# Performance work log

Measured on AMD Instinct MI355X. Metric: run time of the kernel, lower is better.

## Reference

```python
import jax, jax.numpy as jnp
import numpy as np

B, T, D = 16, 1024, 768
H = 12
HD = D // H
MLP = 3072


def _layernorm(x, g, b, eps=1e-5):
    mu = jnp.mean(x, axis=-1, keepdims=True)
    var = jnp.var(x, axis=-1, keepdims=True)
    return (x - mu) * jax.lax.rsqrt(var + eps) * g + b


def setup_inputs() -> dict:
    key = jax.random.key(0)
    ks = jax.random.split(key, 12)
    s_d = 1.0 / np.sqrt(D)
    s_m = 1.0 / np.sqrt(MLP)
    return {
        "x": jax.random.normal(ks[0], (B, T, D), dtype=jnp.float32),
        "Wq": jax.random.uniform(ks[1], (D, D), jnp.float32, -s_d, s_d),
        "bq": jnp.zeros((D,), jnp.float32),
        "Wk": jax.random.uniform(ks[2], (D, D), jnp.float32, -s_d, s_d),
        "bk": jnp.zeros((D,), jnp.float32),
        "Wv": jax.random.uniform(ks[3], (D, D), jnp.float32, -s_d, s_d),
        "bv": jnp.zeros((D,), jnp.float32),
        "Wo": jax.random.uniform(ks[4], (D, D), jnp.float32, -s_d, s_d),
        "bo": jnp.zeros((D,), jnp.float32),
        "ln1_g": jnp.ones((D,), jnp.float32),
        "ln1_b": jnp.zeros((D,), jnp.float32),
        "ln2_g": jnp.ones((D,), jnp.float32),
        "ln2_b": jnp.zeros((D,), jnp.float32),
        "W1": jax.random.uniform(ks[5], (D, MLP), jnp.float32, -s_d, s_d),
        "b1": jnp.zeros((MLP,), jnp.float32),
        "W2": jax.random.uniform(ks[6], (MLP, D), jnp.float32, -s_m, s_m),
        "b2": jnp.zeros((D,), jnp.float32),
    }


def reference(x, Wq, bq, Wk, bk, Wv, bv, Wo, bo, ln1_g, ln1_b, ln2_g, ln2_b, W1, b1, W2, b2):
    h = _layernorm(x, ln1_g, ln1_b)
    # QKV projections -> [B, H, T, HD]
    q = (h @ Wq + bq).reshape(B, T, H, HD).transpose(0, 2, 1, 3)
    k = (h @ Wk + bk).reshape(B, T, H, HD).transpose(0, 2, 1, 3)
    v = (h @ Wv + bv).reshape(B, T, H, HD).transpose(0, 2, 1, 3)
    # NOTE: original divides by sqrt(input_dim), not sqrt(head_dim)
    scores = jnp.einsum('bhtf,bhjf->bhtj', q, k) / jnp.sqrt(jnp.float32(D))
    score = jax.nn.softmax(scores, axis=-1)
    attn = jnp.einsum('bhij,bhjf->bihf', score, v)  # [B, T, H, HD]
    attn_out = attn.reshape(B, T, D) @ Wo + bo
    out = attn_out + x
    h2 = _layernorm(out, ln2_g, ln2_b)
    # MLP: Linear -> GELU -> Linear -> GELU (GELU after 2nd linear is in the source)
    m = jax.nn.gelu(h2 @ W1 + b1, approximate=False)
    m = jax.nn.gelu(m @ W2 + b2, approximate=False)
    return m + out
```

## Files before the change

### kernel.cpp

```cpp
#include <hip/hip_runtime.h>
#include <hip/hip_bf16.h>
#include <math.h>

#define D_MODEL 768
#define T_SEQ   1024
#define B_BATCH 16
#define MLP_DIM 3072
#define M_ROWS  (B_BATCH * T_SEQ)

typedef __attribute__((ext_vector_type(8))) __bf16          bf16x8;
typedef __attribute__((ext_vector_type(4))) __bf16          bf16x4;
typedef __attribute__((ext_vector_type(4))) float           f32x4;

__device__ __forceinline__ float bf2f(unsigned short u) {
  union { unsigned int u; float f; } w; w.u = ((unsigned int)u) << 16; return w.f;
}
__device__ __forceinline__ unsigned short f2bf(float f) {
  union { float f; unsigned int u; } w; w.f = f;
  unsigned int r = (w.u + 0x7fffu + ((w.u >> 16) & 1u)) >> 16;
  return (unsigned short)r;
}
__device__ __forceinline__ float gelu_f(float x) {
  const float a2 = -2.302283f, b2 = -0.102947f;
  return x / (1.0f + exp2f(x * fmaf(b2, x * x, a2)));
}
__device__ __forceinline__ void gload16(const void* g, void* l) {
  __builtin_amdgcn_global_load_lds(
      (const __attribute__((address_space(1))) unsigned int*)g,
      (__attribute__((address_space(3))) unsigned int*)l, 16, 0, 0);
}

__global__ void wtr_k(const float* __restrict__ src,
                      unsigned short* __restrict__ dst, int R, int C) {
  __shared__ float t[32][33];
  const int c0 = blockIdx.x * 32, r0 = blockIdx.y * 32;
  const int tx = threadIdx.x, ty = threadIdx.y;
  #pragma unroll
  for (int j = 0; j < 32; j += 8)
    t[ty + j][tx] = src[(size_t)(r0 + ty + j) * C + (c0 + tx)];
  __syncthreads();
  #pragma unroll
  for (int j = 0; j < 32; j += 8)
    dst[(size_t)(c0 + ty + j) * R + (r0 + tx)] = f2bf(t[tx][ty + j]);
}

__global__ void bcat_k(const float* __restrict__ a, const float* __restrict__ b,
                       const float* __restrict__ c, float* __restrict__ o) {
  const int i = blockIdx.x * 256 + threadIdx.x;
  if (i < 768) { o[i] = a[i]; o[i + 768] = b[i]; o[i + 1536] = c[i]; }
}

template<int SRC_F32>
__global__ __launch_bounds__(256) void ln_k(const void* __restrict__ src,
    const float* __restrict__ g, const float* __restrict__ b,
    unsigned short* __restrict__ out) {
  const int row = blockIdx.x, tid = threadIdx.x;
  const size_t base = (size_t)row * D_MODEL;
  float v[3];
  #pragma unroll
  for (int i = 0; i < 3; ++i) {
    const int c = tid + (i << 8);
    v[i] = SRC_F32 ? ((const float*)src)[base + c]
                   : bf2f(((const unsigned short*)src)[base + c]);
  }
  float s  = v[0] + v[1] + v[2];
  float sq = v[0]*v[0] + v[1]*v[1] + v[2]*v[2];
  #pragma unroll
  for (int m = 32; m; m >>= 1) { s += __shfl_xor(s, m); sq += __shfl_xor(sq, m); }
  __shared__ float ps[4], pq[4];
  if ((tid & 63) == 0) { ps[tid >> 6] = s; pq[tid >> 6] = sq; }
  __syncthreads();
  s  = ps[0] + ps[1] + ps[2] + ps[3];
  sq = pq[0] + pq[1] + pq[2] + pq[3];
  const float mu  = s * (1.0f / 768.0f);
  const float var = sq * (1.0f / 768.0f) - mu * mu;
  const float inv = rsqrtf(var + 1e-5f);
  #pragma unroll
  for (int i = 0; i < 3; ++i) {
    const int c = tid + (i << 8);
    out[base + c] = f2bf((v[i] - mu) * inv * g[c] + b[c]);
  }
}

template<int EP>
__global__ __launch_bounds__(512) void gemm_k(
    const unsigned short* __restrict__ Au, const unsigned short* __restrict__ Btu,
    const float* __restrict__ bias, void* __restrict__ outv,
    const void* __restrict__ residv, void* __restrict__ aux,
    int M, int N, int K, int cgrp) {
  __shared__ __align__(16) __bf16 SMEM[2 * 32768];
  const __bf16* A  = (const __bf16*)Au;
  const __bf16* Bt = (const __bf16*)Btu;
  const int tid = threadIdx.x;
  const int lane = tid & 63, w = tid >> 6;
  const int wr = w >> 2, wc = w & 3;
  const int lr = lane & 15, lg = lane >> 4;
  const int gx = gridDim.x;
  const int bid = blockIdx.y * gx + blockIdx.x;
  const int xcd = bid & 7, idx = bid >> 3;
  const int rpx = gx >> 3;
  const int gsz = rpx * cgrp;
  const int grp = idx / gsz, rem = idx - grp * gsz;
  const int rb = rem / cgrp, cc2 = rem - rb * cgrp + grp * cgrp;
  const int brow = (xcd * rpx + rb) * 256;
  const int bcol = cc2 * 256;

  f32x4 acc[8][4];
  #pragma unroll
  for (int m = 0; m < 8; ++m)
    #pragma unroll
    for (int n = 0; n < 4; ++n) acc[m][n] = (f32x4){0.f, 0.f, 0.f, 0.f};

  const int rrs = lane >> 2;
  const int ccs = (lane & 3) << 3;
  const int csw = ccs ^ ((((lane >> 3) & 3)) << 3);
  const __bf16* sA[4]; const __bf16* sB[4]; int dA[4], dB[4];
  #pragma unroll
  for (int g = 0; g < 4; ++g) {
    const int s = g * 8 + w;
    const int rsrc = (s >> 1) * 16 + rrs;
    const int csrc = (s & 1) * 32 + csw;
    sA[g] = A  + (size_t)(brow + rsrc) * K + csrc;
    sB[g] = Bt + (size_t)(bcol + rsrc) * K + csrc;
    dA[g] = s * 512;
    dB[g] = 16384 + s * 512;
  }

#define STAGE2_(nbb_, k0_, g_) do {                         \
    gload16(sA[g_] + (k0_), &SMEM[(nbb_) + dA[g_]]);        \
    gload16(sB[g_] + (k0_), &SMEM[(nbb_) + dB[g_]]);        \
  } while (0)

  const int rbase = lr * 32 + ((lg << 3) ^ (((lr >> 1) & 3) << 3));

  #pragma unroll
  for (int g = 0; g < 4; ++g) STAGE2_(0, 0, g);

  int cur = 0;
  for (int k0 = 0; k0 < K; k0 += 64, cur ^= 1) {
    const int bb  = cur * 32768;
    const int nbb = (cur ^ 1) * 32768;
    const bool pf = (k0 + 64 < K);
    bf16x8 af0[4][2], af1[4][2], bfr[4][2];
    if (pf) {
      STAGE2_(nbb, k0 + 64, 0);
      asm volatile("s_waitcnt vmcnt(2)" ::: "memory");
    } else {
      asm volatile("s_waitcnt vmcnt(0)" ::: "memory");
    }
    __builtin_amdgcn_s_barrier();
    __builtin_amdgcn_sched_barrier(0);
    #pragma unroll
    for (int ml = 0; ml < 4; ++ml)
      #pragma unroll
      for (int kk = 0; kk < 2; ++kk)
        af0[ml][kk] = *(const bf16x8*)(&SMEM[bb + ((wr*8 + ml)*2 + kk)*512 + rbase]);
    #pragma unroll
    for (int n = 0; n < 2; ++n)
      #pragma unroll
      for (int kk = 0; kk < 2; ++kk)
        bfr[n][kk] = *(const bf16x8*)(&SMEM[bb + 16384 + ((wc*4 + n)*2 + kk)*512 + rbase]);
    asm volatile("s_waitcnt lgkmcnt(0)" ::: "memory");
    __builtin_amdgcn_sched_barrier(0);
    __builtin_amdgcn_s_setprio(1);
    #pragma unroll
    for (int ml = 0; ml < 4; ++ml)
      #pragma unroll
      for (int n = 0; n < 2; ++n) {
        acc[ml][n] = __builtin_amdgcn_mfma_f32_16x16x32_bf16(af0[ml][0], bfr[n][0], acc[ml][n], 0, 0, 0);
        acc[ml][n] = __builtin_amdgcn_mfma_f32_16x16x32_bf16(af0[ml][1], bfr[n][1], acc[ml][n], 0, 0, 0);
      }
    __builtin_amdgcn_s_setprio(0);
    __builtin_amdgcn_s_barrier();
    #pragma unroll
    for (int n = 2; n < 4; ++n)
      #pragma unroll
      for (int kk = 0; kk < 2; ++kk)
        bfr[n][kk] = *(const bf16x8*)(&SMEM[bb + 16384 + ((wc*4 + n)*2 + kk)*512 + rbase]);
    if (pf) STAGE2_(nbb, k0 + 64, 1);
    asm volatile("s_waitcnt lgkmcnt(0)" ::: "memory");
    __builtin_amdgcn_sched_barrier(0);
    __builtin_amdgcn_s_setprio(1);
    #pragma unroll
    for (int ml = 0; ml < 4; ++ml)
      #pragma unroll
      for (int n = 2; n < 4; ++n) {
        acc[ml][n] = __builtin_amdgcn_mfma_f32_16x16x32_bf16(af0[ml][0], bfr[n][0], acc[ml][n], 0, 0, 0);
        acc[ml][n] = __builtin_amdgcn_mfma_f32_16x16x32_bf16(af0[ml][1], bfr[n][1], acc[ml][n], 0, 0, 0);
      }
    __builtin_amdgcn_s_setprio(0);
    __builtin_amdgcn_s_barrier();
    #pragma unroll
    for (int ml = 0; ml < 4; ++ml)
      #pragma unroll
      for (int kk = 0; kk < 2; ++kk)
        af1[ml][kk] = *(const bf16x8*)(&SMEM[bb + ((wr*8 + 4 + ml)*2 + kk)*512 + rbase]);
    if (pf) STAGE2_(nbb, k0 + 64, 2);
    asm volatile("s_waitcnt lgkmcnt(0)" ::: "memory");
    __builtin_amdgcn_sched_barrier(0);
    __builtin_amdgcn_s_setprio(1);
    #pragma unroll
    for (int ml = 0; ml < 4; ++ml)
      #pragma unroll
      for (int n = 0; n < 2; ++n) {
        acc[4+ml][n] = __builtin_amdgcn_mfma_f32_16x16x32_bf16(af1[ml][0], bfr[n][0], acc[4+ml][n], 0, 0, 0);
        acc[4+ml][n] = __builtin_amdgcn_mfma_f32_16x16x32_bf16(af1[ml][1], bfr[n][1], acc[4+ml][n], 0, 0, 0);
      }
    __builtin_amdgcn_s_setprio(0);
    __builtin_amdgcn_s_barrier();
    if (pf) STAGE2_(nbb, k0 + 64, 3);
    __builtin_amdgcn_s_setprio(1);
    #pragma unroll
    for (int ml = 0; ml < 4; ++ml)
      #pragma unroll
      for (int n = 2; n < 4; ++n) {
        acc[4+ml][n] = __builtin_amdgcn_mfma_f32_16x16x32_bf16(af1[ml][0], bfr[n][0], acc[4+ml][n], 0, 0, 0);
        acc[4+ml][n] = __builtin_amdgcn_mfma_f32_16x16x32_bf16(af1[ml][1], bfr[n][1], acc[4+ml][n], 0, 0, 0);
      }
    __builtin_amdgcn_s_setprio(0);
    __builtin_amdgcn_s_barrier();
  }
#undef STAGE2_

  const int seg = (EP == 5) ? (bcol / 768) : 0;
  unsigned short* qkvp = nullptr;
  if (EP == 5)
    qkvp = (seg == 0) ? (unsigned short*)outv
         : (seg == 1) ? (unsigned short*)residv : (unsigned short*)aux;

  if (EP == 5 && seg == 2) {
    #pragma unroll
    for (int n = 0; n < 4; ++n) {
      const int col = bcol + wc*64 + n*16 + lr;
      const float bv = bias[col];
      const int colLv = col - 1536;
      #pragma unroll
      for (int m = 0; m < 8; ++m) {
        const int row0 = brow + wr*128 + m*16 + lg*4;
        #pragma unroll
        for (int r2 = 0; r2 < 4; ++r2) {
          const int gr = row0 + r2;
          qkvp[(((size_t)(gr >> 10) * D_MODEL + colLv) << 10) + (gr & 1023)] =
              f2bf(acc[m][n][r2] + bv);
        }
      }
    }
  } else {
    float* Ep = (float*)SMEM + w * 1280;
    #pragma unroll
    for (int m = 0; m < 8; ++m) {
      #pragma unroll
      for (int n = 0; n < 4; ++n) {
        const int col = bcol + wc*64 + n*16 + lr;
        const float bv = bias[col];
        f32x4 st;
        #pragma unroll
        for (int r2 = 0; r2 < 4; ++r2) {
          float v = acc[m][n][r2] + bv;
          if (EP == 1 || EP == 3) v = gelu_f(v);
          st[r2] = v;
        }
        *(f32x4*)(Ep + (n*16 + lr) * 20 + lg*4) = st;
      }
      #pragma unroll
      for (int i2 = 0; i2 < 2; ++i2) {
        const int rowL = i2*8 + (lane >> 3);
        const int colL = (lane & 7) * 8;
        const int grow = brow + wr*128 + m*16 + rowL;
        const int gcol = bcol + wc*64 + colL;
        float v[8];
        #pragma unroll
        for (int j = 0; j < 8; ++j) v[j] = Ep[(colL + j) * 20 + rowL];
        const size_t o = (size_t)grow * N + gcol;
        if (EP == 3) {
          const bf16x8 rv = *(const bf16x8*)((const __bf16*)residv + o);
          float* op = (float*)outv + o;
          float4 o0, o1;
          o0.x = v[0] + (float)rv[0]; o0.y = v[1] + (float)rv[1];
          o0.z = v[2] + (float)rv[2]; o0.w = v[3] + (float)rv[3];
          o1.x = v[4] + (float)rv[4]; o1.y = v[5] + (float)rv[5];
          o1.z = v[6] + (float)rv[6]; o1.w = v[7] + (float)rv[7];
          *(float4*)op = o0; *(float4*)(op + 4) = o1;
        } else if (EP == 2) {
          const float* rp = (const float*)residv + o;
          const float4 r0 = *(const float4*)rp, r1 = *(const float4*)(rp + 4);
          bf16x8 ov;
          ov[0] = (__bf16)(v[0] + r0.x); ov[1] = (__bf16)(v[1] + r0.y);
          ov[2] = (__bf16)(v[2] + r0.z); ov[3] = (__bf16)(v[3] + r0.w);
          ov[4] = (__bf16)(v[4] + r1.x); ov[5] = (__bf16)(v[5] + r1.y);
          ov[6] = (__bf16)(v[6] + r1.z); ov[7] = (__bf16)(v[7] + r1.w);
          *(bf16x8*)((__bf16*)outv + o) = ov;
        } else if (EP == 5) {
          bf16x8 ov;
          #pragma unroll
          for (int j = 0; j < 8; ++j) ov[j] = (__bf16)v[j];
          *(bf16x8*)((__bf16*)qkvp + (size_t)grow * 768 + (gcol - seg * 768)) = ov;
        } else {
          bf16x8 ov;
          #pragma unroll
          for (int j = 0; j < 8; ++j) ov[j] = (__bf16)v[j];
          *(bf16x8*)((__bf16*)outv + o) = ov;
        }
      }
    }
  }
}

__global__ __launch_bounds__(512) void attn_k(
    const unsigned short* qu, const unsigned short* __restrict__ ku,
    const unsigned short* __restrict__ vtu, unsigned short* attn) {
  __shared__ __align__(16) __bf16 Kl[64][72];
  __shared__ __align__(16) __bf16 Vl[64][72];
  __shared__ __align__(16) __bf16 Pl[8][16][72];
  const __bf16* qg  = (const __bf16*)qu;
  const __bf16* kg  = (const __bf16*)ku;
  const __bf16* vtg = (const __bf16*)vtu;
  const int bid = blockIdx.x;
  const int xcd = bid & 7, idx = bid >> 3;
  const int bh = xcd * 24 + (idx >> 2);
  const int b = bh / 12, h = bh % 12;
  const int q0 = (idx & 3) * 256;
  const int tid = threadIdx.x, lane = tid & 63, w = tid >> 6;
  const int lr = lane & 15, lg = lane >> 4;
  const float scale = 0.03608439182435161f;

  bf16x8 qa[2][2];
  #pragma unroll
  for (int g = 0; g < 2; ++g) {
    const int qrow = b * T_SEQ + q0 + w * 32 + g * 16 + lr;
    const __bf16* qp = qg + (size_t)qrow * D_MODEL + h * 64 + lg * 8;
    qa[g][0] = *(const bf16x8*)(qp);
    qa[g][1] = *(const bf16x8*)(qp + 32);
  }

  const __bf16* kb = kg  + (size_t)b * T_SEQ * D_MODEL + h * 64;
  const __bf16* vb = vtg + ((size_t)b * D_MODEL + h * 64) * T_SEQ;

  f32x4 o[2][4];
  float m_run[2] = {-1e30f, -1e30f}, l_run[2] = {0.f, 0.f};
  #pragma unroll
  for (int g = 0; g < 2; ++g)
    #pragma unroll
    for (int m = 0; m < 4; ++m) o[g][m] = (f32x4){0.f, 0.f, 0.f, 0.f};

  for (int kv0 = 0; kv0 < T_SEQ; kv0 += 64) {
    __syncthreads();
    {
      const int r = tid >> 3, c = (tid & 7) << 3;
      *(bf16x8*)(&Kl[r][c]) = *(const bf16x8*)(kb + (size_t)(kv0 + r) * D_MODEL + c);
      *(bf16x8*)(&Vl[r][c]) = *(const bf16x8*)(vb + (size_t)r * T_SEQ + kv0 + c);
    }
    __syncthreads();

    #pragma unroll
    for (int g = 0; g < 2; ++g) {
      f32x4 s[4];
      __builtin_amdgcn_s_setprio(1);
      #pragma unroll
      for (int m = 0; m < 4; ++m) {
        s[m] = (f32x4){0.f, 0.f, 0.f, 0.f};
        const bf16x8 kf0 = *(const bf16x8*)(&Kl[m*16 + lr][lg*8]);
        const bf16x8 kf1 = *(const bf16x8*)(&Kl[m*16 + lr][32 + lg*8]);
        s[m] = __builtin_amdgcn_mfma_f32_16x16x32_bf16(kf0, qa[g][0], s[m], 0, 0, 0);
        s[m] = __builtin_amdgcn_mfma_f32_16x16x32_bf16(kf1, qa[g][1], s[m], 0, 0, 0);
      }
      __builtin_amdgcn_s_setprio(0);
      float sv[4][4], tm = -1e30f;
      #pragma unroll
      for (int m = 0; m < 4; ++m)
        #pragma unroll
        for (int r = 0; r < 4; ++r) {
          sv[m][r] = s[m][r] * scale;
          tm = fmaxf(tm, sv[m][r]);
        }
      tm = fmaxf(tm, __shfl_xor(tm, 16));
      tm = fmaxf(tm, __shfl_xor(tm, 32));
      const float mn = fmaxf(m_run[g], tm);
      const float sc = __expf(m_run[g] - mn);
      float ts = 0.f;
      bf16x4 pk[4];
      #pragma unroll
      for (int m = 0; m < 4; ++m)
        #pragma unroll
        for (int r = 0; r < 4; ++r) {
          const float pp = __expf(sv[m][r] - mn);
          ts += pp;
          pk[m][r] = (__bf16)pp;
        }
      ts += __shfl_xor(ts, 16);
      ts += __shfl_xor(ts, 32);
      l_run[g] = l_run[g] * sc + ts;
      m_run[g] = mn;
      #pragma unroll
      for (int m = 0; m < 4; ++m)
        #pragma unroll
        for (int r = 0; r < 4; ++r) o[g][m][r] *= sc;
      #pragma unroll
      for (int m = 0; m < 4; ++m)
        *(bf16x4*)(&Pl[w][lr][16*m + 4*lg]) = pk[m];
      const bf16x8 pf0 = *(const bf16x8*)(&Pl[w][lr][lg*8]);
      const bf16x8 pf1 = *(const bf16x8*)(&Pl[w][lr][32 + lg*8]);
      __builtin_amdgcn_s_setprio(1);
      #pragma unroll
      for (int m = 0; m < 4; ++m) {
        const bf16x8 vf0 = *(const bf16x8*)(&Vl[m*16 + lr][lg*8]);
        const bf16x8 vf1 = *(const bf16x8*)(&Vl[m*16 + lr][32 + lg*8]);
        o[g][m] = __builtin_amdgcn_mfma_f32_16x16x32_bf16(vf0, pf0, o[g][m], 0, 0, 0);
        o[g][m] = __builtin_amdgcn_mfma_f32_16x16x32_bf16(vf1, pf1, o[g][m], 0, 0, 0);
      }
      __builtin_amdgcn_s_setprio(0);
    }
  }

  #pragma unroll
  for (int g = 0; g < 2; ++g) {
    const float inv = 1.0f / l_run[g];
    const int qrow = b * T_SEQ + q0 + w * 32 + g * 16 + lr;
    unsigned short* op = attn + (size_t)qrow * D_MODEL + h * 64;
    #pragma unroll
    for (int m = 0; m < 4; ++m) {
      bf16x4 ov;
      #pragma unroll
      for (int r = 0; r < 4; ++r) ov[r] = (__bf16)(o[g][m][r] * inv);
      *(bf16x4*)(op + 16*m + 4*lg) = ov;
    }
  }
}

extern "C" void kernel_launch(void* const* d_in, const int* in_sizes, int n_in,
                              void* d_out, int out_size, void* d_ws, size_t ws_size,
                              hipStream_t stream) {
  const float* x   = (const float*)d_in[0];
  const float* Wq  = (const float*)d_in[1];
  const float* bq  = (const float*)d_in[2];
  const float* Wk  = (const float*)d_in[3];
  const float* bk  = (const float*)d_in[4];
  const float* Wv  = (const float*)d_in[5];
  const float* bv  = (const float*)d_in[6];
  const float* Wo  = (const float*)d_in[7];
  const float* bo  = (const float*)d_in[8];
  const float* g1  = (const float*)d_in[9];
  const float* bt1 = (const float*)d_in[10];
  const float* g2  = (const float*)d_in[11];
  const float* bt2 = (const float*)d_in[12];
  const float* W1  = (const float*)d_in[13];
  const float* bb1 = (const float*)d_in[14];
  const float* W2  = (const float*)d_in[15];
  const float* bb2 = (const float*)d_in[16];

  const size_t SZ = (size_t)M_ROWS * D_MODEL * 2;
  char* wp = (char*)d_ws;
  unsigned short* wqkvT = (unsigned short*)wp; wp += (size_t)2304 * 768 * 2;
  unsigned short* woT   = (unsigned short*)wp; wp += (size_t)768 * 768 * 2;
  unsigned short* w1T   = (unsigned short*)wp; wp += (size_t)768 * 3072 * 2;
  unsigned short* w2T   = (unsigned short*)wp; wp += (size_t)768 * 3072 * 2;
  float*          bqkv  = (float*)wp;          wp += ((size_t)2304 * 4 + 255) & ~(size_t)255;
  unsigned short* kbuf  = (unsigned short*)wp; wp += SZ;
  unsigned short* vtb   = (unsigned short*)wp;
  unsigned short* res2  = kbuf;
  unsigned short* hid   = vtb;
  const size_t avail = ws_size - (size_t)(wp - (char*)d_ws);
  const int nch = (avail >= (size_t)M_ROWS * MLP_DIM * 2) ? 1
                : (avail >= (size_t)(M_ROWS / 2) * MLP_DIM * 2) ? 2 : 4;

  unsigned short* qd = (unsigned short*)d_out;
  unsigned short* h1 = qd + (size_t)M_ROWS * D_MODEL;
  unsigned short* h2 = h1;

  const dim3 tb(32, 8, 1);
  wtr_k<<<dim3(24, 24), tb, 0, stream>>>(Wq, wqkvT, 768, 768);
  wtr_k<<<dim3(24, 24), tb, 0, stream>>>(Wk, wqkvT + (size_t)768 * 768, 768, 768);
  wtr_k<<<dim3(24, 24), tb, 0, stream>>>(Wv, wqkvT + (size_t)1536 * 768, 768, 768);
  wtr_k<<<dim3(24, 24), tb, 0, stream>>>(Wo, woT, 768, 768);
  wtr_k<<<dim3(96, 24), tb, 0, stream>>>(W1, w1T, 768, 3072);
  wtr_k<<<dim3(24, 96), tb, 0, stream>>>(W2, w2T, 3072, 768);
  bcat_k<<<3, 256, 0, stream>>>(bq, bk, bv, bqkv);

  ln_k<1><<<M_ROWS, 256, 0, stream>>>(x, g1, bt1, h1);

  gemm_k<5><<<dim3(64, 9), 512, 0, stream>>>(h1, wqkvT, bqkv, qd, kbuf, vtb,
                                             M_ROWS, 2304, 768, 9);

  attn_k<<<dim3(768), 512, 0, stream>>>(qd, kbuf, vtb, qd);

  gemm_k<2><<<dim3(64, 3), 512, 0, stream>>>(qd, woT, bo, res2, x, nullptr,
                                             M_ROWS, 768, 768, 3);

  ln_k<0><<<M_ROWS, 256, 0, stream>>>(res2, g2, bt2, h2);

  const int CH = M_ROWS / nch;
  for (int c = 0; c < nch; ++c) {
    const size_t ro = (size_t)c * CH;
    gemm_k<1><<<dim3(CH / 256, 12), 512, 0, stream>>>(h2 + ro * 768, w1T, bb1,
        hid, nullptr, nullptr, CH, 3072, 768, 6);
    gemm_k<3><<<dim3(CH / 256, 3), 512, 0, stream>>>(hid, w2T, bb2,
        (float*)d_out + ro * 768, res2 + ro * 768, nullptr, CH, 768, 3072, 3);
  }
}
```

Measured before the change: 487.1 us.

## Add 128x128-tile GEMM kernel for narrow-N output projection and MLP down-projection

Introduces a smaller-tile GEMM variant (128x128 tiles, 256 threads, double-buffered LDS with async global loads) and uses it for the N=768 GEMMs: the attention output projection and the second MLP linear. The previous 256-row tiles launched only 192 blocks (or fewer per chunk) for these GEMMs, which underfills the GPU. Smaller tiles give four times as many blocks, improving occupancy and load balance, at the cost of less data reuse per block and more global traffic.

```diff
diff --git a/kernel.cpp b/kernel.cpp
--- a/kernel.cpp
+++ b/kernel.cpp
@@ -257,7 +257,7 @@
         #pragma unroll
         for (int r2 = 0; r2 < 4; ++r2) {
           float v = acc[m][n][r2] + bv;
-          if (EP == 1 || EP == 3) v = gelu_f(v);
+          if (EP == 1) v = gelu_f(v);
           st[r2] = v;
         }
         *(f32x4*)(Ep + (n*16 + lr) * 20 + lg*4) = st;
@@ -272,25 +272,7 @@
         #pragma unroll
         for (int j = 0; j < 8; ++j) v[j] = Ep[(colL + j) * 20 + rowL];
         const size_t o = (size_t)grow * N + gcol;
-        if (EP == 3) {
-          const bf16x8 rv = *(const bf16x8*)((const __bf16*)residv + o);
-          float* op = (float*)outv + o;
-          float4 o0, o1;
-          o0.x = v[0] + (float)rv[0]; o0.y = v[1] + (float)rv[1];
-          o0.z = v[2] + (float)rv[2]; o0.w = v[3] + (float)rv[3];
-          o1.x = v[4] + (float)rv[4]; o1.y = v[5] + (float)rv[5];
-          o1.z = v[6] + (float)rv[6]; o1.w = v[7] + (float)rv[7];
-          *(float4*)op = o0; *(float4*)(op + 4) = o1;
-        } else if (EP == 2) {
-          const float* rp = (const float*)residv + o;
-          const float4 r0 = *(const float4*)rp, r1 = *(const float4*)(rp + 4);
-          bf16x8 ov;
-          ov[0] = (__bf16)(v[0] + r0.x); ov[1] = (__bf16)(v[1] + r0.y);
-          ov[2] = (__bf16)(v[2] + r0.z); ov[3] = (__bf16)(v[3] + r0.w);
-          ov[4] = (__bf16)(v[4] + r1.x); ov[5] = (__bf16)(v[5] + r1.y);
-          ov[6] = (__bf16)(v[6] + r1.z); ov[7] = (__bf16)(v[7] + r1.w);
-          *(bf16x8*)((__bf16*)outv + o) = ov;
-        } else if (EP == 5) {
+        if (EP == 5) {
           bf16x8 ov;
           #pragma unroll
           for (int j = 0; j < 8; ++j) ov[j] = (__bf16)v[j];
@@ -301,6 +283,125 @@
           for (int j = 0; j < 8; ++j) ov[j] = (__bf16)v[j];
           *(bf16x8*)((__bf16*)outv + o) = ov;
         }
+      }
+    }
+  }
+}
+
+template<int EP>
+__global__ __launch_bounds__(256) void gemm_s(
+    const unsigned short* __restrict__ Au, const unsigned short* __restrict__ Btu,
+    const float* __restrict__ bias, void* __restrict__ outv,
+    const void* __restrict__ residv, int M, int N, int K, int cgrp) {
+  __shared__ __align__(16) __bf16 SMEM[2 * 2 * 128 * 32];
+  auto As = (__bf16 (*)[128][32])(SMEM);
+  auto Bs = (__bf16 (*)[128][32])(SMEM + 2 * 128 * 32);
+  const __bf16* A  = (const __bf16*)Au;
+  const __bf16* Bt = (const __bf16*)Btu;
+  const int tid = threadIdx.x;
+  const int lane = tid & 63, wid = tid >> 6;
+  const int wr = wid >> 1, wc = wid & 1;
+  const int gx = gridDim.x;
+  const int bid = blockIdx.y * gx + blockIdx.x;
+  const int xcd = bid & 7, idx = bid >> 3;
+  const int rpx = gx >> 3;
+  const int gsz = rpx * cgrp;
+  const int grp = idx / gsz, rem = idx - grp * gsz;
+  const int rb = rem / cgrp, cc2 = rem - rb * cgrp + grp * cgrp;
+  const int brow = (xcd * rpx + rb) * 128;
+  const int bcol = cc2 * 128;
+  const int lr = lane & 15, lg = lane >> 4;
+  f32x4 acc[4][4];
+  #pragma unroll
+  for (int m = 0; m < 4; ++m)
+    #pragma unroll
+    for (int n = 0; n < 4; ++n) acc[m][n] = (f32x4){0.f, 0.f, 0.f, 0.f};
+
+  const int srow = (wid << 5) + (lane >> 2);
+  const int scol = (lane & 3) << 3;
+  const __bf16* gA = A  + (size_t)(brow + srow) * K + scol;
+  const __bf16* gB = Bt + (size_t)(bcol + srow) * K + scol;
+
+#define STAGE_(buf_, k0_) do {                                        \
+    gload16(gA + (k0_),                   &As[buf_][(wid << 5)][0]);  \
+    gload16(gA + (k0_) + 16 * (size_t)K,  &As[buf_][(wid << 5) + 16][0]); \
+    gload16(gB + (k0_),                   &Bs[buf_][(wid << 5)][0]);  \
+    gload16(gB + (k0_) + 16 * (size_t)K,  &Bs[buf_][(wid << 5) + 16][0]); \
+  } while (0)
+
+  STAGE_(0, 0);
+  int cur = 0;
+  for (int k0 = 0; k0 < K; k0 += 32, cur ^= 1) {
+    if (k0 + 32 < K) {
+      STAGE_(cur ^ 1, k0 + 32);
+      asm volatile("s_waitcnt vmcnt(4)" ::: "memory");
+    } else {
+      asm volatile("s_waitcnt vmcnt(0)" ::: "memory");
+    }
+    __builtin_amdgcn_s_barrier();
+    __builtin_amdgcn_sched_barrier(0);
+    bf16x8 af[4], bfr[4];
+    #pragma unroll
+    for (int m = 0; m < 4; ++m) af[m]  = *(const bf16x8*)(&As[cur][wr*64 + m*16 + lr][lg*8]);
+    #pragma unroll
+    for (int n = 0; n < 4; ++n) bfr[n] = *(const bf16x8*)(&Bs[cur][wc*64 + n*16 + lr][lg*8]);
+    asm volatile("s_waitcnt lgkmcnt(0)" ::: "memory");
+    __builtin_amdgcn_sched_barrier(0);
+    __builtin_amdgcn_s_setprio(1);
+    #pragma unroll
+    for (int m = 0; m < 4; ++m)
+      #pragma unroll
+      for (int n = 0; n < 4; ++n)
+        acc[m][n] = __builtin_amdgcn_mfma_f32_16x16x32_bf16(af[m], bfr[n], acc[m][n], 0, 0, 0);
+    __builtin_amdgcn_s_setprio(0);
+    __builtin_amdgcn_s_barrier();
+  }
+#undef STAGE_
+
+  float* Ep = (float*)SMEM + wid * 1280;
+  #pragma unroll
+  for (int p = 0; p < 4; ++p) {
+    #pragma unroll
+    for (int n = 0; n < 4; ++n) {
+      const int col = bcol + wc*64 + n*16 + lr;
+      const float bv = bias[col];
+      f32x4 st;
+      #pragma unroll
+      for (int r2 = 0; r2 < 4; ++r2) {
+        float v = acc[p][n][r2] + bv;
+        if (EP == 3) v = gelu_f(v);
+        st[r2] = v;
+      }
+      *(f32x4*)(Ep + (n*16 + lr) * 20 + lg*4) = st;
+    }
+    #pragma unroll
+    for (int i2 = 0; i2 < 2; ++i2) {
+      const int rowL = i2*8 + (lane >> 3);
+      const int colL = (lane & 7) * 8;
+      const int grow = brow + wr*64 + p*16 + rowL;
+      const int gcol = bcol + wc*64 + colL;
+      float v[8];
+      #pragma unroll
+      for (int j = 0; j < 8; ++j) v[j] = Ep[(colL + j) * 20 + rowL];
+      const size_t o = (size_t)grow * N + gcol;
+      if (EP == 3) {
+        const bf16x8 rv = *(const bf16x8*)((const __bf16*)residv + o);
+        float* op = (float*)outv + o;
+        float4 o0, o1;
+        o0.x = v[0] + (float)rv[0]; o0.y = v[1] + (float)rv[1];
+        o0.z = v[2] + (float)rv[2]; o0.w = v[3] + (float)rv[3];
+        o1.x = v[4] + (float)rv[4]; o1.y = v[5] + (float)rv[5];
+        o1.z = v[6] + (float)rv[6]; o1.w = v[7] + (float)rv[7];
+        *(float4*)op = o0; *(float4*)(op + 4) = o1;
+      } else {
+        const float* rp = (const float*)residv + o;
+        const float4 r0 = *(const float4*)rp, r1 = *(const float4*)(rp + 4);
+        bf16x8 ov;
+        ov[0] = (__bf16)(v[0] + r0.x); ov[1] = (__bf16)(v[1] + r0.y);
+        ov[2] = (__bf16)(v[2] + r0.z); ov[3] = (__bf16)(v[3] + r0.w);
+        ov[4] = (__bf16)(v[4] + r1.x); ov[5] = (__bf16)(v[5] + r1.y);
+        ov[6] = (__bf16)(v[6] + r1.z); ov[7] = (__bf16)(v[7] + r1.w);
+        *(bf16x8*)((__bf16*)outv + o) = ov;
       }
     }
   }
@@ -483,8 +584,8 @@
 
   attn_k<<<dim3(768), 512, 0, stream>>>(qd, kbuf, vtb, qd);
 
-  gemm_k<2><<<dim3(64, 3), 512, 0, stream>>>(qd, woT, bo, res2, x, nullptr,
-                                             M_ROWS, 768, 768, 3);
+  gemm_s<2><<<dim3(128, 6), 256, 0, stream>>>(qd, woT, bo, res2, x,
+                                              M_ROWS, 768, 768, 3);
 
   ln_k<0><<<M_ROWS, 256, 0, stream>>>(res2, g2, bt2, h2);
 
@@ -493,7 +594,7 @@
     const size_t ro = (size_t)c * CH;
     gemm_k<1><<<dim3(CH / 256, 12), 512, 0, stream>>>(h2 + ro * 768, w1T, bb1,
         hid, nullptr, nullptr, CH, 3072, 768, 6);
-    gemm_k<3><<<dim3(CH / 256, 3), 512, 0, stream>>>(hid, w2T, bb2,
-        (float*)d_out + ro * 768, res2 + ro * 768, nullptr, CH, 768, 3072, 3);
-  }
-}
+    gemm_s<3><<<dim3(CH / 128, 6), 256, 0, stream>>>(hid, w2T, bb2,
+        (float*)d_out + ro * 768, res2 + ro * 768, CH, 768, 3072, 3);
+  }
+}
```

New measurement: 513.0 us. +5.3%, slower.
